# Kernel optimization log

Hardware: AMD Instinct MI355X
Metric: run time of the kernel (lower is better)

The kernel has to match this reference:

```python
import jax, jax.numpy as jnp
import numpy as np

N = 262144
D_IN, D_OUT, D_H, N_LAYERS = 3, 3, 128, 8


def _linear_init(key, fan_in, fan_out):
    # torch nn.Linear default: U(-1/sqrt(fan_in), 1/sqrt(fan_in)) for W and b
    kw, kb = jax.random.split(key)
    bound = 1.0 / np.sqrt(fan_in)
    W = jax.random.uniform(kw, (fan_out, fan_in), jnp.float32, -bound, bound)
    b = jax.random.uniform(kb, (fan_out,), jnp.float32, -bound, bound)
    return W, b


def setup_inputs() -> dict:
    key = jax.random.key(0)
    keys = jax.random.split(key, N_LAYERS + 2)
    x = jax.random.normal(keys[0], (N, D_IN), jnp.float32)
    W0, b0 = _linear_init(keys[1], D_IN, D_H)
    Wh_list, bh_list = [], []
    for i in range(N_LAYERS - 1):  # 7 hidden linears
        W, b = _linear_init(keys[2 + i], D_H, D_H)
        Wh_list.append(W)
        bh_list.append(b)
    Wh = jnp.stack(Wh_list)          # [7, 128, 128]
    bh = jnp.stack(bh_list)          # [7, 128]
    Wout, bout = _linear_init(keys[N_LAYERS + 1], D_H, D_OUT)
    return {"x": x, "W0": W0, "b0": b0, "Wh": Wh, "bh": bh,
            "Wout": Wout, "bout": bout}


def reference(x, W0, b0, Wh, bh, Wout, bout):
    h = jax.nn.relu(x @ W0.T + b0)                  # [N, 128]
    for i in range(Wh.shape[0]):                    # 7 fixed hidden layers
        h = jax.nn.relu(h @ Wh[i].T + bh[i])
    return h @ Wout.T + bout                        # [N, 3]
```

## Files before the change

kernel.cpp:

```cpp
#include <hip/hip_runtime.h>


typedef __attribute__((ext_vector_type(8)))  _Float16 f16x8;
typedef __attribute__((ext_vector_type(16))) float    floatx16;

#define NLAYERS     9
#define LAYER_H     16384
#define BIAS_FLOATS 1152
#define WG_THREADS  256
#define PTS_PER_WG  256

__global__ void pack_weights(const float* __restrict__ W0, const float* __restrict__ b0,
                             const float* __restrict__ Wh, const float* __restrict__ bhid,
                             const float* __restrict__ Wout, const float* __restrict__ bout,
                             unsigned short* __restrict__ Wpack, float* __restrict__ bias_pack)
{
    const int t = blockIdx.x * 256 + threadIdx.x;
    const int WTOT = NLAYERS * 2048;
    if (t < WTOT) {
        const int lane = t & 63;
        const int ks   = (t >> 6) & 7;
        const int m    = (t >> 9) & 3;
        const int L    = t >> 11;
        const int row  = 32 * m + (lane & 31);
        const int g    = lane >> 5;
        unsigned int ov[4];
        for (int jj = 0; jj < 4; ++jj) {
            unsigned int pair = 0u;
            for (int e = 0; e < 2; ++e) {
                const int j = jj * 2 + e;
                const int k = ks * 16 + 4 * g + (j & 3) + 8 * (j >> 2);
                float w = 0.0f;
                if (L == 0)      { if (k < 3)   w = W0[row * 3 + k]; }
                else if (L < 8)  {              w = Wh[(L - 1) * 16384 + row * 128 + k]; }
                else             { if (row < 3) w = Wout[row * 128 + k]; }
                const _Float16 h = (_Float16)w;
                const unsigned short bits = __builtin_bit_cast(unsigned short, h);
                pair |= ((unsigned int)bits) << (16 * e);
            }
            ov[jj] = pair;
        }
        reinterpret_cast<uint4*>(Wpack)[t] = make_uint4(ov[0], ov[1], ov[2], ov[3]);
    } else if (t < WTOT + BIAS_FLOATS) {
        const int i   = t - WTOT;
        const int idx = i & 15;
        const int g   = (i >> 4) & 1;
        const int m   = (i >> 5) & 3;
        const int L   = i >> 7;
        const int row = 32 * m + (idx & 3) + 8 * (idx >> 2) + 4 * g;
        float v = 0.0f;
        if (L == 0)       v = b0[row];
        else if (L < 8)   v = bhid[(L - 1) * 128 + row];
        else if (row < 3) v = bout[row];
        bias_pack[i] = v;
    }
}

__device__ __forceinline__ void stage32k(const void* src, void* dst, int tid)
{
#pragma unroll
    for (int k = 0; k < 8; ++k) {
        const int off = tid * 16 + k * 4096;
        __builtin_amdgcn_global_load_lds(
            (const __attribute__((address_space(1))) unsigned int*)((const char*)src + off),
            (__attribute__((address_space(3))) unsigned int*)((char*)dst + off),
            16, 0, 0);
    }
}

#define SPLIT1(accv, bv)                                                        \
    _Pragma("unroll")                                                           \
    for (int m = 0; m < 4; ++m) {                                               \
        f16x8 h0, h1;                                                           \
        _Pragma("unroll")                                                       \
        for (int j = 0; j < 8; ++j) {                                           \
            h0[j] = (_Float16)fmaxf(accv[m][j], 0.0f);                          \
            h1[j] = (_Float16)fmaxf(accv[m][j + 8], 0.0f);                      \
        }                                                                       \
        bv[2 * m]     = h0;                                                     \
        bv[2 * m + 1] = h1;                                                     \
    }

__device__ __forceinline__ floatx16 bias_init(const float* blds, int L, int m, int g)
{
    const float4* bp = (const float4*)&blds[((L * 4 + m) * 2 + g) * 16];
    const float4 b0v = bp[0], b1v = bp[1], b2v = bp[2], b3v = bp[3];
    floatx16 a;
    a[0] = b0v.x;  a[1] = b0v.y;  a[2] = b0v.z;  a[3] = b0v.w;
    a[4] = b1v.x;  a[5] = b1v.y;  a[6] = b1v.z;  a[7] = b1v.w;
    a[8] = b2v.x;  a[9] = b2v.y;  a[10] = b2v.z; a[11] = b2v.w;
    a[12] = b3v.x; a[13] = b3v.y; a[14] = b3v.z; a[15] = b3v.w;
    return a;
}

__global__ __launch_bounds__(WG_THREADS, 2) void mlp_fused(
    const float* __restrict__ x, const unsigned short* __restrict__ Wpack,
    const float* __restrict__ bias_pack, float* __restrict__ out)
{
    __shared__ unsigned short Wlds[2][LAYER_H];
    __shared__ float blds[BIAS_FLOATS];

    const int tid  = threadIdx.x;
    const int lane = tid & 63;
    const int wv   = tid >> 6;
    const int col  = lane & 31;
    const int g    = lane >> 5;
    const long pt  = (long)blockIdx.x * PTS_PER_WG + wv * 64 + col;

    for (int i = tid; i < BIAS_FLOATS; i += WG_THREADS) blds[i] = bias_pack[i];
    stage32k(Wpack, &Wlds[0][0], tid);

    f16x8 b1[8], b2[8];
    {
        f16x8 z1 = {(_Float16)0, (_Float16)0, (_Float16)0, (_Float16)0,
                    (_Float16)0, (_Float16)0, (_Float16)0, (_Float16)0};
        f16x8 z2 = z1;
        if (g == 0) {
            const float* xp1 = x + pt * 3;
            const float* xp2 = x + (pt + 32) * 3;
#pragma unroll
            for (int c = 0; c < 3; ++c) {
                z1[c] = (_Float16)xp1[c];
                z2[c] = (_Float16)xp2[c];
            }
        }
        b1[0] = z1;
        b2[0] = z2;
    }
    __syncthreads();

    floatx16 acc[4], acc2[4];

    stage32k(Wpack + LAYER_H, &Wlds[1][0], tid);
#pragma unroll
    for (int m = 0; m < 4; ++m) {
        acc[m]  = bias_init(blds, 0, m, g);
        acc2[m] = acc[m];
    }
#pragma unroll
    for (int m = 0; m < 4; ++m) {
        const f16x8 a = *(const f16x8*)&Wlds[0][(m * 8 + 0) * 512 + lane * 8];
        acc[m]  = __builtin_amdgcn_mfma_f32_32x32x16_f16(a, b1[0], acc[m],  0, 0, 0);
        acc2[m] = __builtin_amdgcn_mfma_f32_32x32x16_f16(a, b2[0], acc2[m], 0, 0, 0);
    }
    SPLIT1(acc, b1)
    SPLIT1(acc2, b2)
    __syncthreads();

#pragma unroll
    for (int L = 1; L < 8; ++L) {
        const unsigned short* wb = &Wlds[L & 1][0];
        stage32k(Wpack + (L + 1) * LAYER_H, &Wlds[(L + 1) & 1][0], tid);
#pragma unroll
        for (int m = 0; m < 4; ++m) {
            acc[m]  = bias_init(blds, L, m, g);
            acc2[m] = acc[m];
        }
#pragma unroll
        for (int ks = 0; ks < 8; ++ks) {
#pragma unroll
            for (int m = 0; m < 4; ++m) {
                const f16x8 a = *(const f16x8*)&wb[(m * 8 + ks) * 512 + lane * 8];
                acc[m]  = __builtin_amdgcn_mfma_f32_32x32x16_f16(a, b1[ks], acc[m],  0, 0, 0);
                acc2[m] = __builtin_amdgcn_mfma_f32_32x32x16_f16(a, b2[ks], acc2[m], 0, 0, 0);
            }
        }
        SPLIT1(acc, b1)
        SPLIT1(acc2, b2)
        __syncthreads();
    }

    floatx16 o1 = bias_init(blds, 8, 0, g);
    floatx16 o2 = o1;
#pragma unroll
    for (int ks = 0; ks < 8; ++ks) {
        const f16x8 a = *(const f16x8*)&Wlds[0][(0 * 8 + ks) * 512 + lane * 8];
        o1 = __builtin_amdgcn_mfma_f32_32x32x16_f16(a, b1[ks], o1, 0, 0, 0);
        o2 = __builtin_amdgcn_mfma_f32_32x32x16_f16(a, b2[ks], o2, 0, 0, 0);
    }
    if (g == 0) {
        float* op1 = out + pt * 3;
        float* op2 = out + (pt + 32) * 3;
        op1[0] = o1[0]; op1[1] = o1[1]; op1[2] = o1[2];
        op2[0] = o2[0]; op2[1] = o2[1]; op2[2] = o2[2];
    }
}

extern "C" void kernel_launch(void* const* d_in, const int* in_sizes, int n_in,
                              void* d_out, int out_size, void* d_ws, size_t ws_size,
                              hipStream_t stream)
{
    const float* x    = (const float*)d_in[0];
    const float* W0   = (const float*)d_in[1];
    const float* b0   = (const float*)d_in[2];
    const float* Wh   = (const float*)d_in[3];
    const float* bh   = (const float*)d_in[4];
    const float* Wout = (const float*)d_in[5];
    const float* bout = (const float*)d_in[6];
    float* out = (float*)d_out;

    unsigned short* Wpack = (unsigned short*)d_ws;
    float* bias_pack = (float*)((char*)d_ws + NLAYERS * LAYER_H * 2);

    const int N = in_sizes[0] / 3;
    const int packThreads = NLAYERS * 2048 + BIAS_FLOATS;

    hipLaunchKernelGGL(pack_weights, dim3((packThreads + 255) / 256), dim3(256), 0, stream,
                       W0, b0, Wh, bh, Wout, bout, Wpack, bias_pack);
    hipLaunchKernelGGL(mlp_fused, dim3(N / PTS_PER_WG), dim3(WG_THREADS), 0, stream,
                       x, Wpack, bias_pack, out);
}
```

Before: 125.3 us.

## Restage weights into large LDS regions with fewer barriers and coalesced output

Replaces the per-layer double-buffered 32KB weight staging with a large LDS layout. Layer 0, layers 1-3 and the output layer load up front, layer 4 goes to a separate region, and layers 5-7 are reloaded over the layer 1-3 region while layer 4 computes. This cuts the synchronisation points from nine barriers to three. Workgroups double to 512 threads, MFMA loops are wrapped in s_setprio, and output stores are staged through LDS so global writes are coalesced. The trade-offs are much higher LDS use (about 143KB plus biases per block), which limits blocks per CU, and a pack kernel that drops the zero-padded unused K slices of layer 0.

Result: faster. 121.6 us (-3.0%).

```diff
diff --git a/kernel.cpp b/kernel.cpp
--- a/kernel.cpp
+++ b/kernel.cpp
@@ -4,11 +4,23 @@
 typedef __attribute__((ext_vector_type(8)))  _Float16 f16x8;
 typedef __attribute__((ext_vector_type(16))) float    floatx16;
 
-#define NLAYERS     9
-#define LAYER_H     16384
 #define BIAS_FLOATS 1152
-#define WG_THREADS  256
-#define PTS_PER_WG  256
+#define WG_THREADS  512
+#define PTS_PER_WG  512
+
+#define SLOT_L0   0
+#define SLOT_L1   256
+#define SLOT_L4   6400
+#define SLOT_L5   8448
+#define SLOT_L8   14592
+#define SLOTS_W   15104
+#define BIAS_OFF_H 120832
+
+#define OFF_L0  0
+#define OFF_P   2048
+#define OFF_Q   51200
+#define OFF_L8  67584
+#define LDS_W_H 71680
 
 __global__ void pack_weights(const float* __restrict__ W0, const float* __restrict__ b0,
                              const float* __restrict__ Wh, const float* __restrict__ bhid,
@@ -16,33 +28,45 @@
                              unsigned short* __restrict__ Wpack, float* __restrict__ bias_pack)
 {
     const int t = blockIdx.x * 256 + threadIdx.x;
-    const int WTOT = NLAYERS * 2048;
-    if (t < WTOT) {
-        const int lane = t & 63;
-        const int ks   = (t >> 6) & 7;
-        const int m    = (t >> 9) & 3;
-        const int L    = t >> 11;
-        const int row  = 32 * m + (lane & 31);
-        const int g    = lane >> 5;
+    if (t < SLOTS_W) {
+        float wv[8];
+        if (t < SLOT_L1) {
+            const int lane = t & 63, m = t >> 6;
+            const int row = 32 * m + (lane & 31), g = lane >> 5;
+#pragma unroll
+            for (int j = 0; j < 8; ++j) {
+                const int k = 4 * g + (j & 3) + 8 * (j >> 2);
+                wv[j] = (k < 3) ? W0[row * 3 + k] : 0.0f;
+            }
+        } else if (t < SLOT_L8) {
+            const int u = t - SLOT_L1;
+            const int lane = u & 63, ks = (u >> 6) & 7, m = (u >> 9) & 3, L1 = u >> 11;
+            const int row = 32 * m + (lane & 31), g = lane >> 5;
+#pragma unroll
+            for (int j = 0; j < 8; ++j) {
+                const int k = 16 * ks + 4 * g + (j & 3) + 8 * (j >> 2);
+                wv[j] = Wh[L1 * 16384 + row * 128 + k];
+            }
+        } else {
+            const int u = t - SLOT_L8;
+            const int lane = u & 63, ks = u >> 6;
+            const int row = lane & 31, g = lane >> 5;
+#pragma unroll
+            for (int j = 0; j < 8; ++j) {
+                const int k = 16 * ks + 4 * g + (j & 3) + 8 * (j >> 2);
+                wv[j] = (row < 3) ? Wout[row * 128 + k] : 0.0f;
+            }
+        }
         unsigned int ov[4];
+#pragma unroll
         for (int jj = 0; jj < 4; ++jj) {
-            unsigned int pair = 0u;
-            for (int e = 0; e < 2; ++e) {
-                const int j = jj * 2 + e;
-                const int k = ks * 16 + 4 * g + (j & 3) + 8 * (j >> 2);
-                float w = 0.0f;
-                if (L == 0)      { if (k < 3)   w = W0[row * 3 + k]; }
-                else if (L < 8)  {              w = Wh[(L - 1) * 16384 + row * 128 + k]; }
-                else             { if (row < 3) w = Wout[row * 128 + k]; }
-                const _Float16 h = (_Float16)w;
-                const unsigned short bits = __builtin_bit_cast(unsigned short, h);
-                pair |= ((unsigned int)bits) << (16 * e);
-            }
-            ov[jj] = pair;
+            const unsigned short e0 = __builtin_bit_cast(unsigned short, (_Float16)wv[2 * jj]);
+            const unsigned short e1 = __builtin_bit_cast(unsigned short, (_Float16)wv[2 * jj + 1]);
+            ov[jj] = (unsigned int)e0 | ((unsigned int)e1 << 16);
         }
         reinterpret_cast<uint4*>(Wpack)[t] = make_uint4(ov[0], ov[1], ov[2], ov[3]);
-    } else if (t < WTOT + BIAS_FLOATS) {
-        const int i   = t - WTOT;
+    } else if (t < SLOTS_W + BIAS_FLOATS) {
+        const int i   = t - SLOTS_W;
         const int idx = i & 15;
         const int g   = (i >> 4) & 1;
         const int m   = (i >> 5) & 3;
@@ -56,14 +80,15 @@
     }
 }
 
-__device__ __forceinline__ void stage32k(const void* src, void* dst, int tid)
-{
-#pragma unroll
-    for (int k = 0; k < 8; ++k) {
-        const int off = tid * 16 + k * 4096;
+__device__ __forceinline__ void stage_range(const unsigned short* Wpack, unsigned short* Wl,
+                                            int src_slot, int dst_half, int nslots, int tid)
+{
+    const char* gsrc = (const char*)Wpack + (size_t)src_slot * 16;
+    char* ldst = (char*)Wl + (size_t)dst_half * 2;
+    for (int i = tid; i < nslots; i += WG_THREADS) {
         __builtin_amdgcn_global_load_lds(
-            (const __attribute__((address_space(1))) unsigned int*)((const char*)src + off),
-            (__attribute__((address_space(3))) unsigned int*)((char*)dst + off),
+            (const __attribute__((address_space(1))) unsigned int*)(gsrc + i * 16),
+            (__attribute__((address_space(3))) unsigned int*)(ldst + i * 16),
             16, 0, 0);
     }
 }
@@ -93,12 +118,38 @@
     return a;
 }
 
+__device__ __forceinline__ void layer_full(const unsigned short* wb, const float* blds,
+                                           int Lb, int g, int lane,
+                                           f16x8 (&b1)[8], f16x8 (&b2)[8])
+{
+    floatx16 acc[4], acc2[4];
+#pragma unroll
+    for (int m = 0; m < 4; ++m) {
+        acc[m]  = bias_init(blds, Lb, m, g);
+        acc2[m] = acc[m];
+    }
+    __builtin_amdgcn_s_setprio(1);
+#pragma unroll
+    for (int ks = 0; ks < 8; ++ks) {
+#pragma unroll
+        for (int m = 0; m < 4; ++m) {
+            const f16x8 a = *(const f16x8*)&wb[(m * 8 + ks) * 512 + lane * 8];
+            acc[m]  = __builtin_amdgcn_mfma_f32_32x32x16_f16(a, b1[ks], acc[m],  0, 0, 0);
+            acc2[m] = __builtin_amdgcn_mfma_f32_32x32x16_f16(a, b2[ks], acc2[m], 0, 0, 0);
+        }
+    }
+    __builtin_amdgcn_s_setprio(0);
+    SPLIT1(acc, b1)
+    SPLIT1(acc2, b2)
+}
+
 __global__ __launch_bounds__(WG_THREADS, 2) void mlp_fused(
     const float* __restrict__ x, const unsigned short* __restrict__ Wpack,
     const float* __restrict__ bias_pack, float* __restrict__ out)
 {
-    __shared__ unsigned short Wlds[2][LAYER_H];
+    __shared__ unsigned short Wl[LDS_W_H];
     __shared__ float blds[BIAS_FLOATS];
+    __shared__ float bounce[WG_THREADS * 3];
 
     const int tid  = threadIdx.x;
     const int lane = tid & 63;
@@ -107,8 +158,9 @@
     const int g    = lane >> 5;
     const long pt  = (long)blockIdx.x * PTS_PER_WG + wv * 64 + col;
 
+    stage_range(Wpack, Wl, SLOT_L0, OFF_L0, 6400, tid);
+    stage_range(Wpack, Wl, SLOT_L8, OFF_L8, 512, tid);
     for (int i = tid; i < BIAS_FLOATS; i += WG_THREADS) blds[i] = bias_pack[i];
-    stage32k(Wpack, &Wlds[0][0], tid);
 
     f16x8 b1[8], b2[8];
     {
@@ -129,60 +181,68 @@
     }
     __syncthreads();
 
-    floatx16 acc[4], acc2[4];
-
-    stage32k(Wpack + LAYER_H, &Wlds[1][0], tid);
-#pragma unroll
-    for (int m = 0; m < 4; ++m) {
-        acc[m]  = bias_init(blds, 0, m, g);
-        acc2[m] = acc[m];
-    }
-#pragma unroll
-    for (int m = 0; m < 4; ++m) {
-        const f16x8 a = *(const f16x8*)&Wlds[0][(m * 8 + 0) * 512 + lane * 8];
-        acc[m]  = __builtin_amdgcn_mfma_f32_32x32x16_f16(a, b1[0], acc[m],  0, 0, 0);
-        acc2[m] = __builtin_amdgcn_mfma_f32_32x32x16_f16(a, b2[0], acc2[m], 0, 0, 0);
-    }
-    SPLIT1(acc, b1)
-    SPLIT1(acc2, b2)
-    __syncthreads();
-
-#pragma unroll
-    for (int L = 1; L < 8; ++L) {
-        const unsigned short* wb = &Wlds[L & 1][0];
-        stage32k(Wpack + (L + 1) * LAYER_H, &Wlds[(L + 1) & 1][0], tid);
+    stage_range(Wpack, Wl, SLOT_L4, OFF_Q, 2048, tid);
+
+    {
+        floatx16 acc[4], acc2[4];
 #pragma unroll
         for (int m = 0; m < 4; ++m) {
-            acc[m]  = bias_init(blds, L, m, g);
+            acc[m]  = bias_init(blds, 0, m, g);
             acc2[m] = acc[m];
         }
-#pragma unroll
-        for (int ks = 0; ks < 8; ++ks) {
-#pragma unroll
-            for (int m = 0; m < 4; ++m) {
-                const f16x8 a = *(const f16x8*)&wb[(m * 8 + ks) * 512 + lane * 8];
-                acc[m]  = __builtin_amdgcn_mfma_f32_32x32x16_f16(a, b1[ks], acc[m],  0, 0, 0);
-                acc2[m] = __builtin_amdgcn_mfma_f32_32x32x16_f16(a, b2[ks], acc2[m], 0, 0, 0);
-            }
-        }
+        __builtin_amdgcn_s_setprio(1);
+#pragma unroll
+        for (int m = 0; m < 4; ++m) {
+            const f16x8 a = *(const f16x8*)&Wl[OFF_L0 + m * 512 + lane * 8];
+            acc[m]  = __builtin_amdgcn_mfma_f32_32x32x16_f16(a, b1[0], acc[m],  0, 0, 0);
+            acc2[m] = __builtin_amdgcn_mfma_f32_32x32x16_f16(a, b2[0], acc2[m], 0, 0, 0);
+        }
+        __builtin_amdgcn_s_setprio(0);
         SPLIT1(acc, b1)
         SPLIT1(acc2, b2)
-        __syncthreads();
-    }
+    }
+
+#pragma unroll
+    for (int L = 1; L <= 3; ++L)
+        layer_full(&Wl[OFF_P + (L - 1) * 16384], blds, L, g, lane, b1, b2);
+
+    __syncthreads();
+
+    stage_range(Wpack, Wl, SLOT_L5, OFF_P, 6144, tid);
+
+    layer_full(&Wl[OFF_Q], blds, 4, g, lane, b1, b2);
+
+    __syncthreads();
+
+#pragma unroll
+    for (int L = 5; L <= 7; ++L)
+        layer_full(&Wl[OFF_P + (L - 5) * 16384], blds, L, g, lane, b1, b2);
 
     floatx16 o1 = bias_init(blds, 8, 0, g);
     floatx16 o2 = o1;
+    __builtin_amdgcn_s_setprio(1);
 #pragma unroll
     for (int ks = 0; ks < 8; ++ks) {
-        const f16x8 a = *(const f16x8*)&Wlds[0][(0 * 8 + ks) * 512 + lane * 8];
+        const f16x8 a = *(const f16x8*)&Wl[OFF_L8 + ks * 512 + lane * 8];
         o1 = __builtin_amdgcn_mfma_f32_32x32x16_f16(a, b1[ks], o1, 0, 0, 0);
         o2 = __builtin_amdgcn_mfma_f32_32x32x16_f16(a, b2[ks], o2, 0, 0, 0);
     }
-    if (g == 0) {
-        float* op1 = out + pt * 3;
-        float* op2 = out + (pt + 32) * 3;
-        op1[0] = o1[0]; op1[1] = o1[1]; op1[2] = o1[2];
-        op2[0] = o2[0]; op2[1] = o2[1]; op2[2] = o2[2];
+    __builtin_amdgcn_s_setprio(0);
+
+    {
+        const int wb = wv * 192;
+        if (g == 0) {
+            bounce[wb + col * 3 + 0] = o1[0];
+            bounce[wb + col * 3 + 1] = o1[1];
+            bounce[wb + col * 3 + 2] = o1[2];
+            bounce[wb + (32 + col) * 3 + 0] = o2[0];
+            bounce[wb + (32 + col) * 3 + 1] = o2[1];
+            bounce[wb + (32 + col) * 3 + 2] = o2[2];
+        }
+        float* ob = out + (long)blockIdx.x * (PTS_PER_WG * 3) + wb;
+#pragma unroll
+        for (int s = 0; s < 3; ++s)
+            ob[s * 64 + lane] = bounce[wb + s * 64 + lane];
     }
 }
 
@@ -200,10 +260,10 @@
     float* out = (float*)d_out;
 
     unsigned short* Wpack = (unsigned short*)d_ws;
-    float* bias_pack = (float*)((char*)d_ws + NLAYERS * LAYER_H * 2);
+    float* bias_pack = (float*)((char*)d_ws + (size_t)BIAS_OFF_H * 2);
 
     const int N = in_sizes[0] / 3;
-    const int packThreads = NLAYERS * 2048 + BIAS_FLOATS;
+    const int packThreads = SLOTS_W + BIAS_FLOATS;
 
     hipLaunchKernelGGL(pack_weights, dim3((packThreads + 255) / 256), dim3(256), 0, stream,
                        W0, b0, Wh, bh, Wout, bout, Wpack, bias_pack);
```
